# Performance work log

Measured on AMD Instinct MI355X. Metric: run time of the kernel, lower is better.

Reference implementation:

```python
import jax, jax.numpy as jnp
import numpy as np
from jax.scipy.special import logsumexp

DEPTH = 7
LOG_EPS = jnp.float32(-64.0)
EPS = jnp.float32(np.exp(-64.0))


def leaf_interval(depth, start_idx=0):
    if depth == 0:
        return ([start_idx], [start_idx], [], start_idx)
    l_l, l_r, l_adj, last = leaf_interval(depth - 1, start_idx)
    my = last + 1
    r_l, r_r, r_adj, last = leaf_interval(depth - 1, my + 1)
    return ([my] + l_l, [my] + r_r,
            [(l, r) for l in l_r for r in r_l] + l_adj + r_adj, last)


_start, _end, _adj, _ = leaf_interval(DEPTH)
_out_idx = np.array([i for i, _ in _adj], dtype=np.int32)
OUT_UNIQ, OUT_INV = np.unique(_out_idx, return_inverse=True)
IN_IDX = np.array([j for _, j in _adj], dtype=np.int32)
START_IDXS = np.array(_start, dtype=np.int32)
END_IDXS = np.array(_end, dtype=np.int32)
N_STATES = 2 ** (DEPTH + 1) - 1  # 255


def log_safe(x):
    m = x < EPS
    return jnp.where(m, LOG_EPS, jnp.log(jnp.where(m, EPS, x)))


def exp_safe(x):
    m = x < LOG_EPS
    return jnp.where(m, EPS, jnp.exp(jnp.where(m, LOG_EPS, x)))


def setup_inputs() -> dict:
    key = jax.random.key(0)
    k1, k2, k3 = jax.random.split(key, 3)
    V, B, vocab, T = N_STATES, 64, 5000, 50
    log_probs = jax.nn.log_softmax(
        jax.random.normal(k1, (V, B, vocab), dtype=jnp.float32), axis=-1)
    targets = jax.random.randint(k2, (T, B), 0, vocab)
    target_lengths = jax.random.randint(k3, (B,), 1, T + 1)
    return {"log_probs": log_probs, "targets": targets,
            "target_lengths": target_lengths}


def _forward_ctreec(extracted, target_lengths):
    # extracted: [T, B, V] time-major per-state label log-probs
    T, B, V = extracted.shape
    out_uniq = jnp.asarray(OUT_UNIQ)
    out_inv = jnp.asarray(OUT_INV)
    in_idx = jnp.asarray(IN_IDX)
    end_idxs = jnp.asarray(END_IDXS)
    prev0 = jnp.zeros((B, V), jnp.float32).at[:, jnp.asarray(START_IDXS)].set(1.0)
    acc0 = jnp.zeros((B,), jnp.float32)

    def step(carry, xs):
        prev_probs, acc = carry
        elp_t, t = xs
        log_curr = log_safe(prev_probs) + elp_t            # [B, V]
        log_out = log_curr[:, out_uniq]                    # [B, U] unique out nodes
        log_C = logsumexp(log_out, axis=-1, keepdims=True)  # [B, 1]
        outgoing = exp_safe(log_out - log_C)[:, out_inv]   # [B, E] per-edge probs
        end = (t + 1) == target_lengths                    # [B]
        end_vals = logsumexp(log_curr[:, end_idxs], axis=1)
        acc = acc + jnp.where(end, end_vals, 0.0)
        mid = ((t + 1) < target_lengths) & (t < T - 1)
        acc = acc + jnp.where(mid, log_C[:, 0], 0.0)
        # scatter-add outgoing edge mass onto destination nodes
        new_prev = jnp.zeros_like(prev_probs).at[:, in_idx].add(outgoing)
        return (new_prev, acc), None

    (_, acc), _ = jax.lax.scan(step, (prev0, acc0),
                               (extracted, jnp.arange(T)))
    return acc


def reference(log_probs, targets, target_lengths):
    V, B, vocab = log_probs.shape
    # extracted[t, b, v] = log_probs[v, b, targets[t, b]]
    extracted = log_probs[:, jnp.arange(B)[None, :], targets]  # [V, T, B]
    extracted = jnp.transpose(extracted, (1, 2, 0))            # [T, B, V]
    return -_forward_ctreec(extracted, target_lengths)
```

## Files before the change

kernel.cpp:

```cpp
#include <hip/hip_runtime.h>
#include <math.h>


#define TT 50
#define BB 64
#define VOCAB 5000
#define NS 255
#define NSP 256
#define LOG_EPS_F (-64.0f)
#define EPS_F 1.6038109389511818e-28f

__device__ __forceinline__ float wred_sum(float x) {
#pragma unroll
    for (int m = 32; m >= 1; m >>= 1) x += __shfl_xor(x, m);
    return x;
}

__global__ __launch_bounds__(512) void ctreec_fused_lin(
    const float* __restrict__ log_probs,
    const int* __restrict__ targets,
    const int* __restrict__ target_lengths,
    float* __restrict__ out)
{
    const int b = blockIdx.x;
    const int tid = threadIdx.x;

    __shared__ float e_lds[TT * NSP];
    __shared__ float outv[NSP];
    __shared__ int tgts[TT];

    const int len = target_lengths[b];

    if (tid < TT) tgts[tid] = targets[tid * BB + b];
    __syncthreads();

    {
        const int v = tid & (NSP - 1);
        const int th = tid >> 8;
        if (v < NS) {
            const float* row =
                log_probs + (size_t)v * (BB * VOCAB) + (size_t)b * VOCAB;
            for (int t = th; t < len; t += 2)
                e_lds[t * NSP + v] = __expf(row[tgts[t]]);
        } else {
            for (int t = th; t < len; t += 2)
                e_lds[t * NSP + v] = 0.0f;
        }
    }
    __syncthreads();

    if (tid >= 64) return;

    const int lane = tid;
    const int vbase = lane * 4;

    bool isend[4], isout[4];
    int kk[4], jj[4];
    float prev[4];
#pragma unroll
    for (int i = 0; i < 4; ++i) {
        int v = vbase + i;
        int p = v + 1;
        bool valid = (v < NS);
        bool pw2 = (p & (p - 1)) == 0;
        bool e_ = valid && ((p + (p & (-p))) == 256);
        isend[i] = e_;
        isout[i] = valid && !e_;
        prev[i] = (valid && pw2) ? 1.0f : 0.0f;
        if (valid && !pw2) {
            int s = __ffs(p) - 1;
            int q = p & (p - 1);
            kk[i] = __ffs(q) - 1;
            jj[i] = v - (1 << s);
        } else { kk[i] = 0; jj[i] = 0; }
    }

    const float4* ev = (const float4*)e_lds;
    float acc = 0.0f;
    float4 eA = ev[lane];
    for (int t = 0; t < len; ++t) {
        float4 cur = eA;
        if (t + 1 < len) eA = ev[(t + 1) * 64 + lane];

        float c[4];
        c[0] = prev[0] * cur.x;
        c[1] = prev[1] * cur.y;
        c[2] = prev[2] * cur.z;
        c[3] = prev[3] * cur.w;

        if (t == len - 1) {
            float s = 0.0f;
#pragma unroll
            for (int i = 0; i < 4; ++i)
                if (isend[i]) s += c[i];
            s = wred_sum(s);
            acc += __logf(s);
        } else {
            *(float4*)&outv[vbase] = make_float4(c[0], c[1], c[2], c[3]);
            float s = 0.0f;
#pragma unroll
            for (int i = 0; i < 4; ++i)
                if (isout[i]) s += c[i];
            s = wred_sum(s);
            acc += __logf(s);
            float rinv = 1.0f / s;
            __builtin_amdgcn_wave_barrier();
#pragma unroll
            for (int i = 0; i < 4; ++i) {
                float np_ = 0.0f;
                int bj = jj[i];
                int n = kk[i];
                for (int a = 0; a < n; ++a) np_ += outv[bj - (1 << a)];
                prev[i] = np_ * rinv;
            }
            __builtin_amdgcn_wave_barrier();
        }
    }
    if (lane == 0) out[b] = -acc;
}

extern "C" void kernel_launch(void* const* d_in, const int* in_sizes, int n_in,
                              void* d_out, int out_size, void* d_ws, size_t ws_size,
                              hipStream_t stream) {
    (void)d_ws; (void)ws_size; (void)in_sizes; (void)n_in; (void)out_size;
    const float* log_probs = (const float*)d_in[0];
    const int* targets = (const int*)d_in[1];
    const int* target_lengths = (const int*)d_in[2];
    float* out = (float*)d_out;

    ctreec_fused_lin<<<dim3(BB), dim3(512), 0, stream>>>(
        log_probs, targets, target_lengths, out);
}
```

Before: 454.9 us.

## Split gather into wide parallel kernel and streamline per-batch tree scan

Splits the fused kernel into a gather kernel launched with one block per (batch, time) pair, which writes exp'd label probabilities to workspace in a rank-permuted node order, and a single-wave scan kernel. The scan precomputes LDS source addresses and prefetches rows two steps ahead. It replaces the per-step shuffle reduction with a lagged LDS partial-sum reduction, normalised with rsqrt over two steps. The aim is to spread the latency-bound random gather across many more blocks and to shorten the serial recurrence's critical path. In exchange it adds a second launch and a workspace round-trip, and it falls back to the old kernel if the workspace is too small.

Result: faster. 385.0 us (-15.4%).

```diff
diff --git a/kernel.cpp b/kernel.cpp
--- a/kernel.cpp
+++ b/kernel.cpp
@@ -7,13 +7,194 @@
 #define VOCAB 5000
 #define NS 255
 #define NSP 256
+#define WS_NEEDED ((size_t)BB * TT * NSP * 4)
 #define LOG_EPS_F (-64.0f)
 #define EPS_F 1.6038109389511818e-28f
 
-__device__ __forceinline__ float wred_sum(float x) {
-#pragma unroll
-    for (int m = 32; m >= 1; m >>= 1) x += __shfl_xor(x, m);
-    return x;
+__device__ __forceinline__ int rank_of(int v) {
+    int p = v + 1;
+    if ((p & (p - 1)) == 0) return 247 + (__ffs(p) - 1);
+    int a = __ffs(p) - 1;
+    int q = p & (p - 1);
+    int k = __ffs(q) - 1;
+    int m = p >> (k + 1);
+    int off = 0;
+#pragma unroll
+    for (int kap = 7; kap >= 1; --kap)
+        if (kap > k) off += kap << (7 - kap);
+    return off + m * k + a;
+}
+
+__global__ __launch_bounds__(256) void gather_kernel(
+    const float* __restrict__ log_probs,
+    const int* __restrict__ targets,
+    const int* __restrict__ target_lengths,
+    float* __restrict__ ews)
+{
+    const int bt = blockIdx.x;
+    const int b = bt / TT;
+    const int t = bt % TT;
+    if (t >= target_lengths[b]) return;
+    const int v = threadIdx.x;
+    const int tgt = targets[t * BB + b];
+    float val = 0.0f;
+    int r = 255;
+    if (v < NS) {
+        val = __expf(log_probs[(size_t)v * (BB * VOCAB) + (size_t)b * VOCAB + tgt]);
+        r = rank_of(v);
+    }
+    ews[(size_t)bt * NSP + r] = val;
+}
+
+__global__ __launch_bounds__(64) void scan_kernel(
+    const float* __restrict__ ews,
+    const int* __restrict__ target_lengths,
+    float* __restrict__ out)
+{
+    const int b = blockIdx.x;
+    const int L = threadIdx.x;
+
+    __shared__ __align__(16) float outv[NSP];
+    __shared__ __align__(16) float pb[2][64];
+    __shared__ __align__(16) float gb[2][16];
+    __shared__ int node_of[NSP];
+
+    const int len = target_lengths[b];
+    const float* erow = ews + (size_t)b * TT * NSP;
+
+#pragma unroll
+    for (int i = 0; i < 4; ++i) {
+        int v = 4 * L + i;
+        if (v < NS) node_of[rank_of(v)] = v;
+    }
+    if (L == 0) node_of[255] = NS;
+    __builtin_amdgcn_wave_barrier();
+    __syncthreads();
+
+    int n_[4];
+    n_[0] = node_of[L];       n_[1] = node_of[64 + L];
+    n_[2] = node_of[128 + L]; n_[3] = node_of[192 + L];
+
+    float pm[4], em[4], prev[4];
+    int kk[4], jj[4];
+#pragma unroll
+    for (int i = 0; i < 4; ++i) {
+        int n = n_[i];
+        int p = n + 1;
+        bool valid = (n < NS);
+        bool pw2 = (p & (p - 1)) == 0;
+        bool e_ = valid && ((p + (p & (-p))) == 256);
+        em[i] = e_ ? 1.0f : 0.0f;
+        pm[i] = (valid && !e_) ? 1.0f : 0.0f;
+        prev[i] = (valid && pw2) ? 1.0f : 0.0f;
+        if (valid && !pw2) {
+            int s = __ffs(p) - 1;
+            jj[i] = n - (1 << s);
+            kk[i] = __ffs(p & (p - 1)) - 1;
+        } else { kk[i] = 0; jj[i] = 0; }
+    }
+    int adr0[7], adr1[4], adr2[2], adr3_;
+#pragma unroll
+    for (int a = 0; a < 7; ++a) {
+        int x = jj[0] - (1 << a);
+        adr0[a] = (a < kk[0]) ? rank_of(x < 0 ? 0 : x) : 255;
+    }
+#pragma unroll
+    for (int a = 0; a < 4; ++a) {
+        int x = jj[1] - (1 << a);
+        adr1[a] = (a < kk[1]) ? rank_of(x < 0 ? 0 : x) : 255;
+    }
+#pragma unroll
+    for (int a = 0; a < 2; ++a) {
+        int x = jj[2] - (1 << a);
+        adr2[a] = (a < kk[2]) ? rank_of(x < 0 ? 0 : x) : 255;
+    }
+    {
+        int x = jj[3] - 1;
+        adr3_ = (0 < kk[3]) ? rank_of(x < 0 ? 0 : x) : 255;
+    }
+
+    float acc = 0.0f;
+    float c[4];
+    float rA[4], rB[4];
+    {
+        const float* rp0 = erow;
+        rA[0] = rp0[L]; rA[1] = rp0[64 + L];
+        rA[2] = rp0[128 + L]; rA[3] = rp0[192 + L];
+        const float* rp1 = erow + ((len > 1) ? NSP : 0);
+        rB[0] = rp1[L]; rB[1] = rp1[64 + L];
+        rB[2] = rp1[128 + L]; rB[3] = rp1[192 + L];
+    }
+
+#define PREF(REG, row) do { if ((row) < len) { \
+        const float* _rp = erow + (size_t)(row) * NSP; \
+        REG[0] = _rp[L]; REG[1] = _rp[64 + L]; \
+        REG[2] = _rp[128 + L]; REG[3] = _rp[192 + L]; } } while (0)
+
+#define STEP(tt, PAR, CREG) do { \
+    c[0] = prev[0] * CREG[0]; c[1] = prev[1] * CREG[1]; \
+    c[2] = prev[2] * CREG[2]; c[3] = prev[3] * CREG[3]; \
+    PREF(CREG, (tt) + 2); \
+    if ((tt) == len - 1) goto final_step; \
+    { \
+        float P = (c[0] * pm[0] + c[1] * pm[1]) + (c[2] * pm[2] + c[3] * pm[3]); \
+        outv[L] = c[0]; outv[64 + L] = c[1]; \
+        outv[128 + L] = c[2]; outv[192 + L] = c[3]; \
+        pb[PAR][L] = P; \
+        __builtin_amdgcn_wave_barrier(); \
+        float np0, np1, np2, np3; \
+        { float r0 = outv[adr0[0]], r1 = outv[adr0[1]], r2 = outv[adr0[2]], \
+                r3 = outv[adr0[3]], r4 = outv[adr0[4]], r5 = outv[adr0[5]], \
+                r6 = outv[adr0[6]]; \
+          np0 = ((r0 + r1) + (r2 + r3)) + ((r4 + r5) + r6); } \
+        { float r0 = outv[adr1[0]], r1 = outv[adr1[1]], r2 = outv[adr1[2]], \
+                r3 = outv[adr1[3]]; \
+          np1 = (r0 + r1) + (r2 + r3); } \
+        np2 = outv[adr2[0]] + outv[adr2[1]]; \
+        np3 = outv[adr3_]; \
+        float rinv = 1.0f; \
+        if ((tt) >= 2) { \
+            float4 g0 = *(const float4*)&gb[PAR][0]; \
+            float4 g1 = *(const float4*)&gb[PAR][4]; \
+            float4 g2 = *(const float4*)&gb[PAR][8]; \
+            float4 g3 = *(const float4*)&gb[PAR][12]; \
+            float R = ((((g0.x + g0.y) + (g0.z + g0.w)) + \
+                        ((g1.x + g1.y) + (g1.z + g1.w))) + \
+                       (((g2.x + g2.y) + (g2.z + g2.w)) + \
+                        ((g3.x + g3.y) + (g3.z + g3.w)))); \
+            rinv = rsqrtf(R); \
+            acc += 0.5f * __logf(R); \
+        } \
+        if ((tt) >= 1) { \
+            float4 q = *(const float4*)&pb[PAR ^ 1][4 * (L & 15)]; \
+            gb[PAR ^ 1][L & 15] = (q.x + q.y) + (q.z + q.w); \
+        } \
+        prev[0] = np0 * rinv; prev[1] = np1 * rinv; \
+        prev[2] = np2 * rinv; prev[3] = np3 * rinv; \
+    } \
+} while (0)
+
+    for (int t = 0; ; t += 2) {
+        STEP(t, 0, rA);
+        STEP(t + 1, 1, rB);
+    }
+
+final_step:
+    {
+        float E = (c[0] * em[0] + c[1] * em[1]) + (c[2] * em[2] + c[3] * em[3]);
+        pb[0][L] = E;
+        __builtin_amdgcn_wave_barrier();
+        float tot = 0.0f;
+#pragma unroll
+        for (int g = 0; g < 16; ++g) {
+            float4 q = *(const float4*)&pb[0][4 * g];
+            tot += (q.x + q.y) + (q.z + q.w);
+        }
+        acc += __logf(tot);
+        if (L == 0) out[b] = -acc;
+    }
+#undef STEP
+#undef PREF
 }
 
 __global__ __launch_bounds__(512) void ctreec_fused_lin(
@@ -24,22 +205,17 @@
 {
     const int b = blockIdx.x;
     const int tid = threadIdx.x;
-
     __shared__ float e_lds[TT * NSP];
     __shared__ float outv[NSP];
     __shared__ int tgts[TT];
-
     const int len = target_lengths[b];
-
     if (tid < TT) tgts[tid] = targets[tid * BB + b];
     __syncthreads();
-
     {
         const int v = tid & (NSP - 1);
         const int th = tid >> 8;
         if (v < NS) {
-            const float* row =
-                log_probs + (size_t)v * (BB * VOCAB) + (size_t)b * VOCAB;
+            const float* row = log_probs + (size_t)v * (BB * VOCAB) + (size_t)b * VOCAB;
             for (int t = th; t < len; t += 2)
                 e_lds[t * NSP + v] = __expf(row[tgts[t]]);
         } else {
@@ -48,12 +224,9 @@
         }
     }
     __syncthreads();
-
     if (tid >= 64) return;
-
     const int lane = tid;
     const int vbase = lane * 4;
-
     bool isend[4], isout[4];
     int kk[4], jj[4];
     float prev[4];
@@ -69,39 +242,33 @@
         prev[i] = (valid && pw2) ? 1.0f : 0.0f;
         if (valid && !pw2) {
             int s = __ffs(p) - 1;
-            int q = p & (p - 1);
-            kk[i] = __ffs(q) - 1;
+            kk[i] = __ffs(p & (p - 1)) - 1;
             jj[i] = v - (1 << s);
         } else { kk[i] = 0; jj[i] = 0; }
     }
-
     const float4* ev = (const float4*)e_lds;
     float acc = 0.0f;
     float4 eA = ev[lane];
     for (int t = 0; t < len; ++t) {
         float4 cur = eA;
         if (t + 1 < len) eA = ev[(t + 1) * 64 + lane];
-
-        float c[4];
-        c[0] = prev[0] * cur.x;
-        c[1] = prev[1] * cur.y;
-        c[2] = prev[2] * cur.z;
-        c[3] = prev[3] * cur.w;
-
+        float cc[4];
+        cc[0] = prev[0] * cur.x; cc[1] = prev[1] * cur.y;
+        cc[2] = prev[2] * cur.z; cc[3] = prev[3] * cur.w;
         if (t == len - 1) {
             float s = 0.0f;
 #pragma unroll
-            for (int i = 0; i < 4; ++i)
-                if (isend[i]) s += c[i];
-            s = wred_sum(s);
+            for (int i = 0; i < 4; ++i) if (isend[i]) s += cc[i];
+#pragma unroll
+            for (int m = 32; m >= 1; m >>= 1) s += __shfl_xor(s, m);
             acc += __logf(s);
         } else {
-            *(float4*)&outv[vbase] = make_float4(c[0], c[1], c[2], c[3]);
+            *(float4*)&outv[vbase] = make_float4(cc[0], cc[1], cc[2], cc[3]);
             float s = 0.0f;
 #pragma unroll
-            for (int i = 0; i < 4; ++i)
-                if (isout[i]) s += c[i];
-            s = wred_sum(s);
+            for (int i = 0; i < 4; ++i) if (isout[i]) s += cc[i];
+#pragma unroll
+            for (int m = 32; m >= 1; m >>= 1) s += __shfl_xor(s, m);
             acc += __logf(s);
             float rinv = 1.0f / s;
             __builtin_amdgcn_wave_barrier();
@@ -122,12 +289,20 @@
 extern "C" void kernel_launch(void* const* d_in, const int* in_sizes, int n_in,
                               void* d_out, int out_size, void* d_ws, size_t ws_size,
                               hipStream_t stream) {
-    (void)d_ws; (void)ws_size; (void)in_sizes; (void)n_in; (void)out_size;
+    (void)in_sizes; (void)n_in; (void)out_size;
     const float* log_probs = (const float*)d_in[0];
     const int* targets = (const int*)d_in[1];
     const int* target_lengths = (const int*)d_in[2];
     float* out = (float*)d_out;
 
-    ctreec_fused_lin<<<dim3(BB), dim3(512), 0, stream>>>(
-        log_probs, targets, target_lengths, out);
-}
+    if (ws_size >= WS_NEEDED) {
+        float* ews = (float*)d_ws;
+        gather_kernel<<<dim3(BB * TT), dim3(256), 0, stream>>>(
+            log_probs, targets, target_lengths, ews);
+        scan_kernel<<<dim3(BB), dim3(64), 0, stream>>>(
+            ews, target_lengths, out);
+    } else {
+        ctreec_fused_lin<<<dim3(BB), dim3(512), 0, stream>>>(
+            log_probs, targets, target_lengths, out);
+    }
+}
```
